# Kernel optimization log

Measured on AMD Instinct MI355X. Metric: run time of the kernel, lower is better.

The kernel has to match this reference:

```python
import jax, jax.numpy as jnp
import numpy as np

B, IN_F, OUT_F, GRID = 8192, 1024, 1024, 5


def setup_inputs() -> dict:
    key = jax.random.key(0)
    k1, k2, k3, k4 = jax.random.split(key, 4)
    X = jax.random.normal(k1, (B, IN_F), dtype=jnp.float32)
    # Per-edge linear B-spline coefficients on a uniform grid over [-1, 1]
    coeffs = jax.random.normal(k2, (OUT_F, GRID), dtype=jnp.float32) * 0.1
    # Per-edge 2->1 Linear (PyTorch default init: U(-s, s), s = 1/sqrt(fan_in=2))
    s = 1.0 / np.sqrt(2.0)
    W = jax.random.uniform(k3, (OUT_F, 2), dtype=jnp.float32, minval=-s, maxval=s)
    b = jax.random.uniform(k4, (OUT_F,), dtype=jnp.float32, minval=-s, maxval=s)
    return {"X": X, "coeffs": coeffs, "W": W, "b": b}


def _bspline_linear(x, coeffs):
    # x: [B, O], coeffs: [O, G]. Linear (degree-1) B-spline interpolation on
    # a uniform knot grid over [-1, 1]; x clamped to the grid range.
    G = coeffs.shape[1]
    h = 2.0 / (G - 1)                      # knot spacing
    t = (jnp.clip(x, -1.0, 1.0) + 1.0) / h  # grid coordinate in [0, G-1]
    k = jnp.clip(jnp.floor(t), 0, G - 2).astype(jnp.int32)  # left knot index
    frac = t - k
    e = jnp.arange(coeffs.shape[0])[None, :]  # per-edge row index [1, O]
    c0 = coeffs[e, k]
    c1 = coeffs[e, k + 1]
    return c0 * (1.0 - frac) + c1 * frac


def reference(X, coeffs, W, b):
    # X: [B, in_f]; coeffs: [O, G]; W: [O, 2]; b: [O]  ->  Y: [B, O]
    in_f = X.shape[1]
    O = W.shape[0]
    idx_in = jnp.arange(O) % in_f          # edge i reads input i % in_features
    x = X[:, idx_in]                        # [B, O]
    silu = jax.nn.silu(x)                   # [B, O]
    spline = _bspline_linear(x, coeffs)     # [B, O]
    # Per-edge 2->1 linear combine: Y[:, i] = W[i,0]*silu + W[i,1]*spline + b[i]
    Y = silu * W[:, 0][None, :] + spline * W[:, 1][None, :] + b[None, :]
    return Y
```

## Files before the change

### kernel.cpp

```cpp
#include <hip/hip_runtime.h>
#include <math.h>


#define B_ROWS   8192
#define N_FEAT   1024
#define N_BLOCKS 2048
#define ROWS_PER_BLOCK (B_ROWS / N_BLOCKS)

__global__ __launch_bounds__(256) void kan_kernel(
    const float* __restrict__ X,
    const float* __restrict__ coeffs,
    const float* __restrict__ W,
    const float* __restrict__ bias,
    float* __restrict__ Y)
{
    const int t    = threadIdx.x;
    const int col0 = t * 4;

    float c0[4], d0[4], d1[4], d2[4], d3[4], w0[4], w1[4], bb[4];
#pragma unroll
    for (int j = 0; j < 4; ++j) {
        const int col = col0 + j;
        const float* cp = coeffs + col * 5;
        const float a0 = cp[0], a1 = cp[1], a2 = cp[2], a3 = cp[3], a4 = cp[4];
        c0[j] = a0;
        d0[j] = a1 - a0;
        d1[j] = a2 - a1;
        d2[j] = a3 - a2;
        d3[j] = a4 - a3;
        w0[j] = W[col * 2 + 0];
        w1[j] = W[col * 2 + 1];
        bb[j] = bias[col];
    }

#pragma unroll
    for (int i = 0; i < ROWS_PER_BLOCK; ++i) {
        const int row = blockIdx.x + i * N_BLOCKS;
        const size_t base = (size_t)row * N_FEAT + col0;

        const float4 x4 = *reinterpret_cast<const float4*>(X + base);
        const float xs[4] = {x4.x, x4.y, x4.z, x4.w};
        float ys[4];

#pragma unroll
        for (int j = 0; j < 4; ++j) {
            const float x = xs[j];

            const float sig  = 1.0f / (1.0f + __expf(-x));
            const float silu = x * sig;

            const float xc = fminf(fmaxf(x, -1.0f), 1.0f);
            const float tt = fmaf(2.0f, xc, 2.0f);
            const float r0 = fminf(tt, 1.0f);
            const float r1 = fminf(fmaxf(tt - 1.0f, 0.0f), 1.0f);
            const float r2 = fminf(fmaxf(tt - 2.0f, 0.0f), 1.0f);
            const float r3 = fminf(fmaxf(tt - 3.0f, 0.0f), 1.0f);
            float s = c0[j];
            s = fmaf(d0[j], r0, s);
            s = fmaf(d1[j], r1, s);
            s = fmaf(d2[j], r2, s);
            s = fmaf(d3[j], r3, s);

            ys[j] = fmaf(silu, w0[j], fmaf(s, w1[j], bb[j]));
        }

        *reinterpret_cast<float4*>(Y + base) =
            make_float4(ys[0], ys[1], ys[2], ys[3]);
    }
}

extern "C" void kernel_launch(void* const* d_in, const int* in_sizes, int n_in,
                              void* d_out, int out_size, void* d_ws, size_t ws_size,
                              hipStream_t stream) {
    const float* X      = (const float*)d_in[0];
    const float* coeffs = (const float*)d_in[1];
    const float* W      = (const float*)d_in[2];
    const float* b      = (const float*)d_in[3];
    float* Y            = (float*)d_out;

    kan_kernel<<<N_BLOCKS, 256, 0, stream>>>(X, coeffs, W, b, Y);
}
```

Measured before the change: 91.29 us.

## Stage params in LDS, batch all X loads up front, halve block count

Coefficients, W and bias are copied into shared memory with coalesced float4 loads, replacing strided per-thread global reads. Each block now handles 8 contiguous rows, and all X loads are issued before any compute to raise memory-level parallelism. The grid shrinks to 1024 blocks and launch bounds request 4 blocks per SM. The costs are higher register pressure from buffering 8 float4s and a shared-memory fill plus barrier in every block.

```diff
diff --git a/kernel.cpp b/kernel.cpp
--- a/kernel.cpp
+++ b/kernel.cpp
@@ -4,47 +4,79 @@
 
 #define B_ROWS   8192
 #define N_FEAT   1024
-#define N_BLOCKS 2048
+#define N_BLOCKS 1024
 #define ROWS_PER_BLOCK (B_ROWS / N_BLOCKS)
 
-__global__ __launch_bounds__(256) void kan_kernel(
+__global__ __launch_bounds__(256, 4) void kan_kernel(
     const float* __restrict__ X,
     const float* __restrict__ coeffs,
     const float* __restrict__ W,
     const float* __restrict__ bias,
     float* __restrict__ Y)
 {
-    const int t    = threadIdx.x;
+    __shared__ float s_c[N_FEAT * 5];
+    __shared__ float s_w[N_FEAT * 2];
+    __shared__ float s_b[N_FEAT];
+
+    const int t = threadIdx.x;
+
+    {
+        float4*       dc = reinterpret_cast<float4*>(s_c);
+        const float4* gc = reinterpret_cast<const float4*>(coeffs);
+#pragma unroll
+        for (int u = 0; u < 5; ++u)
+            dc[u * 256 + t] = gc[u * 256 + t];
+
+        float4*       dw = reinterpret_cast<float4*>(s_w);
+        const float4* gw = reinterpret_cast<const float4*>(W);
+#pragma unroll
+        for (int u = 0; u < 2; ++u)
+            dw[u * 256 + t] = gw[u * 256 + t];
+
+        float4*       db = reinterpret_cast<float4*>(s_b);
+        const float4* gb = reinterpret_cast<const float4*>(bias);
+        db[t] = gb[t];
+    }
+    __syncthreads();
+
     const int col0 = t * 4;
-
     float c0[4], d0[4], d1[4], d2[4], d3[4], w0[4], w1[4], bb[4];
 #pragma unroll
     for (int j = 0; j < 4; ++j) {
         const int col = col0 + j;
-        const float* cp = coeffs + col * 5;
-        const float a0 = cp[0], a1 = cp[1], a2 = cp[2], a3 = cp[3], a4 = cp[4];
+        const float a0 = s_c[col * 5 + 0];
+        const float a1 = s_c[col * 5 + 1];
+        const float a2 = s_c[col * 5 + 2];
+        const float a3 = s_c[col * 5 + 3];
+        const float a4 = s_c[col * 5 + 4];
         c0[j] = a0;
         d0[j] = a1 - a0;
         d1[j] = a2 - a1;
         d2[j] = a3 - a2;
         d3[j] = a4 - a3;
-        w0[j] = W[col * 2 + 0];
-        w1[j] = W[col * 2 + 1];
-        bb[j] = bias[col];
+        w0[j] = s_w[col * 2 + 0];
+        w1[j] = s_w[col * 2 + 1];
+        bb[j] = s_b[col];
+    }
+
+    const int row0 = blockIdx.x * ROWS_PER_BLOCK;
+
+    float4 xs[ROWS_PER_BLOCK];
+#pragma unroll
+    for (int i = 0; i < ROWS_PER_BLOCK; ++i) {
+        const size_t base = (size_t)(row0 + i) * N_FEAT + col0;
+        xs[i] = *reinterpret_cast<const float4*>(X + base);
     }
 
 #pragma unroll
     for (int i = 0; i < ROWS_PER_BLOCK; ++i) {
-        const int row = blockIdx.x + i * N_BLOCKS;
-        const size_t base = (size_t)row * N_FEAT + col0;
-
-        const float4 x4 = *reinterpret_cast<const float4*>(X + base);
-        const float xs[4] = {x4.x, x4.y, x4.z, x4.w};
+        const size_t base = (size_t)(row0 + i) * N_FEAT + col0;
+        const float xv[4] = {xs[i].x, xs[i].y, xs[i].z, xs[i].w};
         float ys[4];
 
 #pragma unroll
         for (int j = 0; j < 4; ++j) {
-            const float x = xs[j];
+            const float x = xv[j];
 
             const float sig  = 1.0f / (1.0f + __expf(-x));
             const float silu = x * sig;
```

Result: no change. 90.48 us, median of 2 (-0.9%).
